# Kernel tuning notes

Hardware: AMD Instinct MI355X
Metric: run time of the kernel (lower is better)

## Reference

```python
import jax
import jax.numpy as jnp
from jax import lax
import numpy as np

B, CIN, COUT, RANK, K, H, W = 16, 256, 256, 64, 3, 112, 112
PAD = 1


def setup_inputs() -> dict:
    key = jax.random.key(0)
    k1, k2, k3, k4, k5 = jax.random.split(key, 5)
    x = jax.random.normal(k1, (B, CIN, H, W), dtype=jnp.float32)
    # head: `rank` stacked 1x1 conv weights, each [COUT, CIN]
    w_head = jax.random.normal(k2, (RANK, COUT, CIN), dtype=jnp.float32) * 0.05
    # body: Conv2d(COUT -> RANK, kernel (K,1)), OIHW layout
    w_body = jax.random.normal(k3, (RANK, COUT, K, 1), dtype=jnp.float32) * 0.05
    # tail: Conv2d(RANK -> COUT, kernel (1,K)), OIHW layout, with bias
    w_tail = jax.random.normal(k4, (COUT, RANK, 1, K), dtype=jnp.float32) * 0.05
    b_tail = jax.random.normal(k5, (COUT,), dtype=jnp.float32) * 0.05
    return {"x": x, "w_head": w_head, "w_body": w_body, "w_tail": w_tail, "b_tail": b_tail}


_DN = lax.conv_dimension_numbers((B, CIN, H, W), (COUT, CIN, 1, 1), ("NCHW", "OIHW", "NCHW"))


def reference(x, w_head, w_body, w_tail, b_tail):
    # Sum of rank 1x1 convs over the same input == one 1x1 conv with summed
    # weights (conv is linear in the weight) — same math, one pass.
    w_sum = w_head.sum(axis=0)                      # [COUT, CIN]
    y = jnp.einsum("bihw,oi->bohw", x, w_sum)       # [B, COUT, H, W]
    # body: (K,1) conv, stride (1,1), padding (PAD, 0)
    y = lax.conv_general_dilated(y, w_body, window_strides=(1, 1),
                                 padding=((PAD, PAD), (0, 0)),
                                 dimension_numbers=_DN)  # [B, RANK, H, W]
    # tail: (1,K) conv, stride (1,1), padding (0, PAD), plus bias
    y = lax.conv_general_dilated(y, w_tail, window_strides=(1, 1),
                                 padding=((0, 0), (PAD, PAD)),
                                 dimension_numbers=_DN)  # [B, COUT, H, W]
    return y + b_tail[None, :, None, None]
```

## Files before the change

### kernel.cpp

```cpp
#include <hip/hip_runtime.h>
#include <stdint.h>

#define CIN 256
#define COUT 256
#define RANK 64
#define H_ 112
#define W_ 112
#define HW_ (112*112)

typedef short bf16x8 __attribute__((ext_vector_type(8)));
typedef float f32x4 __attribute__((ext_vector_type(4)));

__device__ __forceinline__ unsigned rne2(float a, float b){
  unsigned ua = __builtin_bit_cast(unsigned, a);
  unsigned ub = __builtin_bit_cast(unsigned, b);
  ua += 0x7FFFu + ((ua >> 16) & 1u);
  ub += 0x7FFFu + ((ub >> 16) & 1u);
  return (ua >> 16) | (ub & 0xFFFF0000u);
}
__device__ __forceinline__ unsigned short rne1(float a){
  unsigned ua = __builtin_bit_cast(unsigned, a);
  ua += 0x7FFFu + ((ua >> 16) & 1u);
  return (unsigned short)(ua >> 16);
}

__global__ __launch_bounds__(256) void k_pre1(const float* __restrict__ x,
                                              unsigned short* __restrict__ xt,
                                              const float* __restrict__ wh,
                                              float* __restrict__ wsum,
                                              int base_b, int nb){
  __shared__ float ldsf[64*120];
  const int tid = threadIdx.x;
  if (blockIdx.x >= (unsigned)(nb*114)){
    int o = blockIdx.x - nb*114;
    float s = 0.f;
    for (int k = 0; k < RANK; ++k) s += wh[(k*COUT + o)*CIN + tid];
    wsum[o*CIN + tid] = s;
    return;
  }
  const int lb = blockIdx.x / 114, hh = blockIdx.x % 114;
  const int bb = base_b + lb;
  const int h = hh - 1;
  unsigned short* dst = xt + ((size_t)(lb*114 + hh))*28672;

  if (h < 0 || h >= H_){
    uint4 z = {0,0,0,0};
    #pragma unroll
    for (int j = 0; j < 14; ++j)
      *(uint4*)(dst + (tid + 256*j)*8) = z;
    return;
  }

  for (int i0p = 0; i0p < 4; ++i0p){
    int c = tid / 28, wq = tid % 28;
    #pragma unroll
    for (int j = 0; j < 7; ++j){
      const float4 v = *(const float4*)(x + ((size_t)(bb*CIN + i0p*64 + c))*HW_ + h*W_ + wq*4);
      *(float4*)&ldsf[c*120 + wq*4] = v;
      wq += 4; c += 9; if (wq >= 28){ wq -= 28; c += 1; }
    }
    __syncthreads();
    for (int ck = tid; ck < 896; ck += 256){
      int g8 = ck / 112, w = ck % 112;
      const float* src = &ldsf[(g8*8)*120 + w];
      uint4 st;
      st.x = rne2(src[0],     src[120]);
      st.y = rne2(src[240],   src[360]);
      st.z = rne2(src[480],   src[600]);
      st.w = rne2(src[720],   src[840]);
      *(uint4*)(dst + (size_t)(i0p*896 + ck)*8) = st;
    }
    __syncthreads();
  }
}

__global__ __launch_bounds__(256) void k_pre2(const float* __restrict__ wb,
                                              const float* __restrict__ wsum,
                                              unsigned short* __restrict__ weff,
                                              const float* __restrict__ wt,
                                              unsigned short* __restrict__ wtp){
  const int tid = threadIdx.x;
  if (blockIdx.x < 192){
    int bid = blockIdx.x;
    int dh = bid >> 6, r = bid & 63;
    float s = 0.f;
    for (int o = 0; o < COUT; ++o)
      s += wb[(r*COUT + o)*3 + dh] * wsum[o*CIN + tid];
    weff[bid*CIN + tid] = rne1(s);
  } else {
    int o = blockIdx.x - 192;
    if (tid < 192){
      int dw = tid >> 6, r = tid & 63;
      wtp[o*192 + tid] = rne1(wt[(o*RANK + r)*3 + dw]);
    }
  }
}

__global__ __launch_bounds__(256,4) void k_fused(const unsigned short* __restrict__ xt,
                                                 const unsigned short* __restrict__ weff,
                                                 const unsigned short* __restrict__ wtp,
                                                 const float* __restrict__ bias,
                                                 float* __restrict__ out,
                                                 int base_b){
  __shared__ alignas(16) unsigned short lds[16416];
  const int tid  = threadIdx.x;
  const int wid  = tid >> 6, lane = tid & 63, g = lane >> 4, l15 = lane & 15;
  const int lb   = blockIdx.x / 56, hb = blockIdx.x % 56;
  const int bb   = base_b + lb;
  const int h0   = hb*2;
  const int hloc = wid >> 1, rhalf = wid & 1;

  f32x4 acc[2][7];
  #pragma unroll
  for (int a = 0; a < 2; ++a)
    #pragma unroll
    for (int b = 0; b < 7; ++b) acc[a][b] = (f32x4){0.f,0.f,0.f,0.f};

  const unsigned short* rowbase = xt + ((size_t)(lb*114 + h0 + wid)*8)*3584;

  auto stage = [&](unsigned short* dstbuf, int q){
    const int i0 = q >> 1, hf = q & 1;
    const unsigned short* src0 = rowbase + (size_t)i0*3584;
    if (hf == 0){
      unsigned short* dstb = dstbuf + wid*2048;
      const unsigned short* s = src0 + lane*8;
      #pragma unroll
      for (int gc = 0; gc < 4; ++gc)
        __builtin_amdgcn_global_load_lds(
          (const __attribute__((address_space(1))) void*)(s + gc*896),
          (__attribute__((address_space(3))) void*)(dstb + gc*512), 16, 0, 0);
    } else {
      if (lane < 48){
        unsigned short* dstb = dstbuf + wid*1536;
        const unsigned short* s = src0 + 512 + lane*8;
        #pragma unroll
        for (int gc = 0; gc < 4; ++gc)
          __builtin_amdgcn_global_load_lds(
            (const __attribute__((address_space(1))) void*)(s + gc*896),
            (__attribute__((address_space(3))) void*)(dstb + gc*384), 16, 0, 0);
      }
    }
  };

  auto compute = [&](const unsigned short* buf, int q){
    const int i0 = q >> 1, hf = q & 1;
    const int wt0 = hf ? 4 : 0, wtn = hf ? 3 : 4;
    const int rstride = hf ? 1536 : 2048;
    const int gstride = hf ? 384 : 512;
    #pragma unroll
    for (int dh = 0; dh < 3; ++dh){
      const unsigned short* ab = weff + (size_t)(dh*64 + rhalf*32 + l15)*CIN + i0*32 + g*8;
      bf16x8 af0 = *(const bf16x8*)(ab);
      bf16x8 af1 = *(const bf16x8*)(ab + 16*CIN);
      const unsigned short* qb = buf + (hloc + dh)*rstride + g*gstride + l15*8;
      #pragma unroll
      for (int w = 0; w < 4; ++w){
        if (w < wtn){
          bf16x8 bfv = *(const bf16x8*)(qb + w*128);
          acc[0][wt0+w] = __builtin_amdgcn_mfma_f32_16x16x32_bf16(af0, bfv, acc[0][wt0+w], 0, 0, 0);
          acc[1][wt0+w] = __builtin_amdgcn_mfma_f32_16x16x32_bf16(af1, bfv, acc[1][wt0+w], 0, 0, 0);
        }
      }
    }
  };

  unsigned short* cur = lds;
  unsigned short* nxt = lds + 8192;
  stage(cur, 0);
  __syncthreads();
  for (int q = 0; q < 16; ++q){
    if (q < 15) stage(nxt, q+1);
    compute(cur, q);
    __syncthreads();
    unsigned short* tmp = cur; cur = nxt; nxt = tmp;
  }

  unsigned short* y2b = lds;
  if (tid < 32){
    int hh = tid >> 4, wsel = (tid >> 3) & 1, rq = tid & 7;
    *(uint4*)(y2b + hh*8208 + (wsel ? 113 : 0)*72 + rq*8) = (uint4){0,0,0,0};
  }
  #pragma unroll
  for (int wt = 0; wt < 7; ++wt){
    #pragma unroll
    for (int rt = 0; rt < 2; ++rt){
      unsigned lo = rne2(acc[rt][wt][0], acc[rt][wt][1]);
      unsigned hi = rne2(acc[rt][wt][2], acc[rt][wt][3]);
      uint2 st; st.x = lo; st.y = hi;
      *(uint2*)(y2b + hloc*8208 + (wt*16 + l15 + 1)*72 + rhalf*32 + rt*16 + g*4) = st;
    }
  }
  __syncthreads();

  const int h = h0 + hloc;
  #pragma unroll
  for (int opass = 0; opass < 4; ++opass){
    const int obase = rhalf*128 + opass*32;
    f32x4 a2[2][7];
    #pragma unroll
    for (int a = 0; a < 2; ++a)
      #pragma unroll
      for (int b = 0; b < 7; ++b) a2[a][b] = (f32x4){0.f,0.f,0.f,0.f};

    #pragma unroll
    for (int s = 0; s < 6; ++s){
      bf16x8 afc[2];
      const unsigned short* ab = wtp + (size_t)(obase + l15)*192 + s*32 + g*8;
      #pragma unroll
      for (int rt = 0; rt < 2; ++rt)
        afc[rt] = *(const bf16x8*)(ab + rt*16*192);
      const unsigned short* qb = y2b + hloc*8208 + (l15 + (s >> 1))*72 + (s & 1)*32 + g*8;
      #pragma unroll
      for (int wt = 0; wt < 7; ++wt){
        bf16x8 bv = *(const bf16x8*)(qb + wt*16*72);
        #pragma unroll
        for (int rt = 0; rt < 2; ++rt)
          a2[rt][wt] = __builtin_amdgcn_mfma_f32_16x16x32_bf16(afc[rt], bv, a2[rt][wt], 0, 0, 0);
      }
    }

    float* ob = out + ((size_t)(bb*COUT) + obase)*HW_ + h*W_;
    #pragma unroll
    for (int rt = 0; rt < 2; ++rt){
      #pragma unroll
      for (int ii = 0; ii < 4; ++ii){
        float bvv = bias[obase + rt*16 + g*4 + ii];
        #pragma unroll
        for (int wt = 0; wt < 7; ++wt)
          ob[(size_t)(rt*16 + g*4 + ii)*HW_ + wt*16 + l15] = a2[rt][wt][ii] + bvv;
      }
    }
  }
}

extern "C" void kernel_launch(void* const* d_in, const int* in_sizes, int n_in,
                              void* d_out, int out_size, void* d_ws, size_t ws_size,
                              hipStream_t stream) {
  const float* x      = (const float*)d_in[0];
  const float* w_head = (const float*)d_in[1];
  const float* w_body = (const float*)d_in[2];
  const float* w_tail = (const float*)d_in[3];
  const float* b_tail = (const float*)d_in[4];
  float* out = (float*)d_out;
  char* ws = (char*)d_ws;

  float*          wsum = (float*)ws;
  unsigned short* weff = (unsigned short*)(ws + 262144);
  unsigned short* wtp  = (unsigned short*)(ws + 360448);
  unsigned short* xt   = (unsigned short*)(ws + 458752);

  const size_t XT_PER_B = (size_t)114 * 57344;
  size_t avail = (ws_size > 458752) ? ws_size - 458752 : 0;
  int chunk_b = (int)(avail / XT_PER_B);
  if (chunk_b > 16) chunk_b = 16;
  if (chunk_b < 1)  chunk_b = 1;
  int nchunks = (16 + chunk_b - 1) / chunk_b;

  int base = 0;
  for (int c = 0; c < nchunks; ++c){
    int remaining = 16 - base;
    int nb = (remaining + (nchunks - c) - 1) / (nchunks - c);
    k_pre1<<<nb*114 + (c == 0 ? 256 : 0), 256, 0, stream>>>(x, xt, w_head, wsum, base, nb);
    if (c == 0)
      k_pre2<<<448, 256, 0, stream>>>(w_body, wsum, weff, w_tail, wtp);
    k_fused<<<nb*56, 256, 0, stream>>>(xt, weff, wtp, b_tail, out, base);
    base += nb;
  }
}
```

Measured before the change: 179.0 us.

## Triple-buffer LDS staging with explicit vmcnt waits and hoisted A-fragment loads

Moves the main loop from double to triple buffering in LDS, so global-to-LDS copies are issued two stages ahead. Each iteration now synchronises with a manual s_waitcnt vmcnt plus s_barrier instead of __syncthreads. The weff A-fragment loads are hoisted and loaded once per pair of half-steps rather than every step. The aim is to hide global load latency and cut redundant loads, at the cost of more LDS per block and a lower launch-bounds occupancy (4 to 3). The hand-tuned vmcnt counts risk a race if the number of outstanding loads differs by lane.

After: 183.9 us. +2.7%, slower.

```diff
diff --git a/kernel.cpp b/kernel.cpp
--- a/kernel.cpp
+++ b/kernel.cpp
@@ -96,13 +96,13 @@
   }
 }
 
-__global__ __launch_bounds__(256,4) void k_fused(const unsigned short* __restrict__ xt,
+__global__ __launch_bounds__(256,3) void k_fused(const unsigned short* __restrict__ xt,
                                                  const unsigned short* __restrict__ weff,
                                                  const unsigned short* __restrict__ wtp,
                                                  const float* __restrict__ bias,
                                                  float* __restrict__ out,
                                                  int base_b){
-  __shared__ alignas(16) unsigned short lds[16416];
+  __shared__ alignas(16) unsigned short lds[24576];
   const int tid  = threadIdx.x;
   const int wid  = tid >> 6, lane = tid & 63, g = lane >> 4, l15 = lane & 15;
   const int lb   = blockIdx.x / 56, hb = blockIdx.x % 56;
@@ -142,38 +142,50 @@
     }
   };
 
-  auto compute = [&](const unsigned short* buf, int q){
-    const int i0 = q >> 1, hf = q & 1;
+  bf16x8 af0[3], af1[3];
+  auto loadA = [&](int i0){
+    #pragma unroll
+    for (int dh = 0; dh < 3; ++dh){
+      const unsigned short* ab = weff + (size_t)(dh*64 + rhalf*32 + l15)*CIN + i0*32 + g*8;
+      af0[dh] = *(const bf16x8*)(ab);
+      af1[dh] = *(const bf16x8*)(ab + 16*CIN);
+    }
+  };
+
+  auto mstep = [&](const unsigned short* buf, int q){
+    const int hf = q & 1;
     const int wt0 = hf ? 4 : 0, wtn = hf ? 3 : 4;
     const int rstride = hf ? 1536 : 2048;
     const int gstride = hf ? 384 : 512;
     #pragma unroll
     for (int dh = 0; dh < 3; ++dh){
-      const unsigned short* ab = weff + (size_t)(dh*64 + rhalf*32 + l15)*CIN + i0*32 + g*8;
-      bf16x8 af0 = *(const bf16x8*)(ab);
-      bf16x8 af1 = *(const bf16x8*)(ab + 16*CIN);
       const unsigned short* qb = buf + (hloc + dh)*rstride + g*gstride + l15*8;
       #pragma unroll
       for (int w = 0; w < 4; ++w){
         if (w < wtn){
           bf16x8 bfv = *(const bf16x8*)(qb + w*128);
-          acc[0][wt0+w] = __builtin_amdgcn_mfma_f32_16x16x32_bf16(af0, bfv, acc[0][wt0+w], 0, 0, 0);
-          acc[1][wt0+w] = __builtin_amdgcn_mfma_f32_16x16x32_bf16(af1, bfv, acc[1][wt0+w], 0, 0, 0);
+          acc[0][wt0+w] = __builtin_amdgcn_mfma_f32_16x16x32_bf16(af0[dh], bfv, acc[0][wt0+w], 0, 0, 0);
+          acc[1][wt0+w] = __builtin_amdgcn_mfma_f32_16x16x32_bf16(af1[dh], bfv, acc[1][wt0+w], 0, 0, 0);
         }
       }
     }
   };
 
-  unsigned short* cur = lds;
-  unsigned short* nxt = lds + 8192;
-  stage(cur, 0);
-  __syncthreads();
+  unsigned short* const bufs[3] = {lds, lds + 8192, lds + 16384};
+  stage(bufs[0], 0);
+  stage(bufs[1], 1);
+  #pragma unroll
   for (int q = 0; q < 16; ++q){
-    if (q < 15) stage(nxt, q+1);
-    compute(cur, q);
-    __syncthreads();
-    unsigned short* tmp = cur; cur = nxt; nxt = tmp;
-  }
+    if (q < 15) asm volatile("s_waitcnt vmcnt(4)" ::: "memory");
+    else        asm volatile("s_waitcnt vmcnt(0)" ::: "memory");
+    __builtin_amdgcn_s_barrier();
+    __builtin_amdgcn_sched_barrier(0);
+    if ((q & 1) == 0) loadA(q >> 1);
+    if (q < 14) stage(bufs[(q + 2) % 3], q + 2);
+    mstep(bufs[q % 3], q);
+  }
+  asm volatile("s_waitcnt vmcnt(0)" ::: "memory");
+  __builtin_amdgcn_s_barrier();
 
   unsigned short* y2b = lds;
   if (tid < 32){
```
